# Kernel tuning notes

Measured on AMD Instinct MI355X. Metric: run time of the kernel, lower is better.

The kernel has to match this reference:

```python
import jax, jax.numpy as jnp
import numpy as np

B, N, D, LAT, EC = 1024, 256, 64, 128, 32


def setup_inputs() -> dict:
    key = jax.random.key(0)
    ks = jax.random.split(key, 8)
    s = lambda d: 1.0 / np.sqrt(d)
    return {
        "local_data": jax.random.normal(ks[0], (B, D), jnp.float32),
        "neighbor_data": jax.random.normal(ks[1], (B, N, D), jnp.float32),
        "Wc": jax.random.normal(ks[2], (D, EC), jnp.float32) * s(D),
        "bc": jnp.zeros((EC,), jnp.float32),
        "Wf": jax.random.normal(ks[3], (D, LAT), jnp.float32) * s(D),
        "bf": jnp.zeros((LAT,), jnp.float32),
        "Wa": jax.random.normal(ks[4], (3 * EC, LAT), jnp.float32) * s(3 * EC),
        "ba": jnp.zeros((LAT,), jnp.float32),
        "Wl": jax.random.normal(ks[5], (LAT, LAT), jnp.float32) * s(LAT),
        "bl": jnp.zeros((LAT,), jnp.float32),
    }


def reference(local_data, neighbor_data, Wc, bc, Wf, bf, Wa, ba, Wl, bl):
    # per-neighbor feature encoder: [B,N,LAT]
    enc_feature = jax.nn.relu(jnp.einsum("bnd,dk->bnk", neighbor_data, Wf) + bf)
    # per-neighbor communication encoder: [B,N,EC]
    enc_comm = jax.nn.relu(jnp.einsum("bnd,dk->bnk", neighbor_data, Wc) + bc)
    # self communication embedding: [B,EC]
    enc_comm_self = jax.nn.relu(local_data @ Wc + bc)
    # broadcast self and neighbor-mean to [B,N,EC]
    self_rep = jnp.broadcast_to(enc_comm_self[:, None, :], enc_comm.shape)
    mean_rep = jnp.broadcast_to(enc_comm.mean(axis=1, keepdims=True), enc_comm.shape)
    cat = jnp.concatenate([self_rep, enc_comm, mean_rep], axis=-1)  # [B,N,3*EC]
    # attention: linear then softmax over neighbor axis (dim=-2)
    att = jax.nn.softmax(jnp.einsum("bnc,ck->bnk", cat, Wa) + ba, axis=1)  # [B,N,LAT]
    # attention-weighted sum over neighbors: [B,LAT]
    aggregated = jnp.einsum("bnk,bnk->bk", att, enc_feature)
    # later layer
    return jax.nn.relu(aggregated @ Wl + bl)
```

## Files before the change

kernel.cpp:

```cpp
#include <hip/hip_runtime.h>

#define NB    256
#define DIN   64
#define LATD  128
#define ECD   32

typedef __attribute__((ext_vector_type(8))) __bf16 bf16x8;
typedef __attribute__((ext_vector_type(4))) float f32x4;
typedef __attribute__((ext_vector_type(4))) unsigned short u16x4;

#define XS_STRIDE 72
#define EC_STRIDE 40
#define WA_STRIDE 40

#define WS_WC 0
#define WS_WF (32 * 72)
#define WS_WA (32 * 72 + 128 * 72)

#define MFMA(a, b, c) __builtin_amdgcn_mfma_f32_16x16x32_bf16((a), (b), (c), 0, 0, 0)

__device__ __forceinline__ unsigned short f2bf(float f) {
    unsigned u = __builtin_bit_cast(unsigned, f);
    u += 0x7fffu + ((u >> 16) & 1u);
    return (unsigned short)(u >> 16);
}

__global__ __launch_bounds__(256) void prep_kernel(
    const float* __restrict__ Wc, const float* __restrict__ Wf,
    const float* __restrict__ Wa, unsigned short* __restrict__ ws)
{
    int t = blockIdx.x * blockDim.x + threadIdx.x;
    int stride = gridDim.x * blockDim.x;
    for (int i = t; i < 32 * 64; i += stride) {
        int n = i >> 6, k = i & 63;
        ws[WS_WC + n * XS_STRIDE + k] = f2bf(Wc[k * ECD + n]);
    }
    for (int i = t; i < 128 * 64; i += stride) {
        int n = i >> 6, k = i & 63;
        ws[WS_WF + n * XS_STRIDE + k] = f2bf(Wf[k * LATD + n]);
    }
    for (int i = t; i < 128 * 32; i += stride) {
        int n = i >> 5, k = i & 31;
        ws[WS_WA + n * WA_STRIDE + k] = f2bf(Wa[(ECD + k) * LATD + n]);
    }
}

__global__ __launch_bounds__(256) void arm_main(
    const float* __restrict__ ld,
    const float* __restrict__ xg,
    const float* __restrict__ wc,
    const float* __restrict__ bcv,
    const float* __restrict__ bfv,
    const float* __restrict__ wa,
    const float* __restrict__ bav,
    const float* __restrict__ wl,
    const float* __restrict__ blv,
    const unsigned short* __restrict__ ws,
    float* __restrict__ out)
{
    __shared__ unsigned short Xs[NB * XS_STRIDE];
    __shared__ unsigned short ecs[NB * EC_STRIDE];
    __shared__ float meanpart[4][ECD];
    __shared__ float mean_s[ECD];
    __shared__ float self_s[ECD];
    __shared__ float c0_s[LATD];
    __shared__ float redmax[4][16];
    __shared__ float redsum[4][16];
    __shared__ float aggpart[4][LATD];
    __shared__ float aggfull[LATD];

    const int b    = blockIdx.x;
    const int tid  = threadIdx.x;
    const int lane = tid & 63;
    const int w    = tid >> 6;
    const int l15  = lane & 15;
    const int q    = lane >> 4;

    {
        const float4* xb4 = reinterpret_cast<const float4*>(xg + (size_t)b * NB * DIN);
        #pragma unroll
        for (int i = 0; i < 16; ++i) {
            int i4 = i * 256 + tid;
            float4 v = xb4[i4];
            int n = i4 >> 4;
            int d = (i4 & 15) << 2;
            u16x4 p = { f2bf(v.x), f2bf(v.y), f2bf(v.z), f2bf(v.w) };
            *reinterpret_cast<u16x4*>(&Xs[n * XS_STRIDE + d]) = p;
        }
    }
    __syncthreads();

    {
        bf16x8 wfrag[2][2];
        #pragma unroll
        for (int ks = 0; ks < 2; ++ks)
            #pragma unroll
            for (int nb = 0; nb < 2; ++nb)
                wfrag[ks][nb] = *reinterpret_cast<const bf16x8*>(
                    &ws[WS_WC + (nb * 16 + l15) * XS_STRIDE + ks * 32 + q * 8]);

        float bc0 = bcv[l15], bc1 = bcv[16 + l15];
        float s0 = 0.f, s1 = 0.f;
        #pragma unroll
        for (int t = 0; t < 4; ++t) {
            int rowA = (w * 4 + t) * 16;
            f32x4 a0 = {0.f, 0.f, 0.f, 0.f}, a1 = {0.f, 0.f, 0.f, 0.f};
            #pragma unroll
            for (int ks = 0; ks < 2; ++ks) {
                bf16x8 af = *reinterpret_cast<const bf16x8*>(
                    &Xs[(rowA + l15) * XS_STRIDE + ks * 32 + q * 8]);
                a0 = MFMA(af, wfrag[ks][0], a0);
                a1 = MFMA(af, wfrag[ks][1], a1);
            }
            #pragma unroll
            for (int r = 0; r < 4; ++r) {
                int row = rowA + q * 4 + r;
                float e0 = fmaxf(a0[r] + bc0, 0.f);
                float e1 = fmaxf(a1[r] + bc1, 0.f);
                ecs[row * EC_STRIDE + l15]      = f2bf(e0);
                ecs[row * EC_STRIDE + 16 + l15] = f2bf(e1);
                s0 += e0; s1 += e1;
            }
        }
        s0 += __shfl_xor(s0, 16, 64); s0 += __shfl_xor(s0, 32, 64);
        s1 += __shfl_xor(s1, 16, 64); s1 += __shfl_xor(s1, 32, 64);
        if (lane < 16) { meanpart[w][lane] = s0; meanpart[w][16 + lane] = s1; }
    }
    __syncthreads();

    if (tid < 32) {
        mean_s[tid] = (meanpart[0][tid] + meanpart[1][tid] +
                       meanpart[2][tid] + meanpart[3][tid]) * (1.f / 256.f);
    } else if (tid < 64) {
        int e = tid - 32;
        float acc = 0.f;
        #pragma unroll 8
        for (int d = 0; d < 64; ++d) acc += ld[b * 64 + d] * wc[d * ECD + e];
        self_s[e] = fmaxf(acc + bcv[e], 0.f);
    }
    __syncthreads();

    if (tid < 128) {
        float acc = bav[tid];
        #pragma unroll 4
        for (int e = 0; e < 32; ++e) {
            acc += self_s[e] * wa[e * LATD + tid];
            acc += mean_s[e] * wa[(64 + e) * LATD + tid];
        }
        c0_s[tid] = acc;
    }
    __syncthreads();

    bf16x8 xfrag[4][2];
    bf16x8 ecfrag[4];
    #pragma unroll
    for (int t = 0; t < 4; ++t) {
        int row = (w * 4 + t) * 16 + l15;
        xfrag[t][0] = *reinterpret_cast<const bf16x8*>(&Xs[row * XS_STRIDE + q * 8]);
        xfrag[t][1] = *reinterpret_cast<const bf16x8*>(&Xs[row * XS_STRIDE + 32 + q * 8]);
        ecfrag[t]   = *reinterpret_cast<const bf16x8*>(&ecs[row * EC_STRIDE + q * 8]);
    }

    for (int g = 0; g < 8; ++g) {
        bf16x8 wf0 = *reinterpret_cast<const bf16x8*>(
            &ws[WS_WF + (g * 16 + l15) * XS_STRIDE + q * 8]);
        bf16x8 wf1 = *reinterpret_cast<const bf16x8*>(
            &ws[WS_WF + (g * 16 + l15) * XS_STRIDE + 32 + q * 8]);
        bf16x8 wag = *reinterpret_cast<const bf16x8*>(
            &ws[WS_WA + (g * 16 + l15) * WA_STRIDE + q * 8]);

        f32x4 ef[4], lg[4];
        #pragma unroll
        for (int t = 0; t < 4; ++t) {
            f32x4 z = {0.f, 0.f, 0.f, 0.f};
            z = MFMA(xfrag[t][0], wf0, z);
            ef[t] = MFMA(xfrag[t][1], wf1, z);
            f32x4 z2 = {0.f, 0.f, 0.f, 0.f};
            lg[t] = MFMA(ecfrag[t], wag, z2);
        }
        float bfl = bfv[g * 16 + l15];
        float c0l = c0_s[g * 16 + l15];
        float mx = -1e30f;
        #pragma unroll
        for (int t = 0; t < 4; ++t)
            #pragma unroll
            for (int r = 0; r < 4; ++r) {
                ef[t][r] = fmaxf(ef[t][r] + bfl, 0.f);
                lg[t][r] += c0l;
                mx = fmaxf(mx, lg[t][r]);
            }
        mx = fmaxf(mx, __shfl_xor(mx, 16, 64));
        mx = fmaxf(mx, __shfl_xor(mx, 32, 64));
        if (lane < 16) redmax[w][lane] = mx;
        __syncthreads();
        mx = fmaxf(fmaxf(redmax[0][l15], redmax[1][l15]),
                   fmaxf(redmax[2][l15], redmax[3][l15]));

        float sm = 0.f;
        #pragma unroll
        for (int t = 0; t < 4; ++t)
            #pragma unroll
            for (int r = 0; r < 4; ++r) {
                float e = exp2f((lg[t][r] - mx) * 1.44269504f);
                lg[t][r] = e;
                sm += e;
            }
        sm += __shfl_xor(sm, 16, 64); sm += __shfl_xor(sm, 32, 64);
        if (lane < 16) redsum[w][lane] = sm;
        __syncthreads();
        sm = redsum[0][l15] + redsum[1][l15] + redsum[2][l15] + redsum[3][l15];
        float inv = 1.0f / sm;

        float ag = 0.f;
        #pragma unroll
        for (int t = 0; t < 4; ++t)
            #pragma unroll
            for (int r = 0; r < 4; ++r)
                ag += lg[t][r] * ef[t][r];
        ag *= inv;
        ag += __shfl_xor(ag, 16, 64);
        ag += __shfl_xor(ag, 32, 64);
        if (lane < 16) aggpart[w][g * 16 + lane] = ag;
    }
    __syncthreads();

    if (tid < 128)
        aggfull[tid] = aggpart[0][tid] + aggpart[1][tid] +
                       aggpart[2][tid] + aggpart[3][tid];
    __syncthreads();
    if (tid < 128) {
        float acc = blv[tid];
        #pragma unroll 8
        for (int k = 0; k < 128; ++k) acc += aggfull[k] * wl[k * LATD + tid];
        out[(size_t)b * LATD + tid] = fmaxf(acc, 0.f);
    }
}

extern "C" void kernel_launch(void* const* d_in, const int* in_sizes, int n_in,
                              void* d_out, int out_size, void* d_ws, size_t ws_size,
                              hipStream_t stream)
{
    const float* ld  = (const float*)d_in[0];
    const float* xg  = (const float*)d_in[1];
    const float* wc  = (const float*)d_in[2];
    const float* bc_ = (const float*)d_in[3];
    const float* wf  = (const float*)d_in[4];
    const float* bf_ = (const float*)d_in[5];
    const float* wa  = (const float*)d_in[6];
    const float* ba_ = (const float*)d_in[7];
    const float* wl  = (const float*)d_in[8];
    const float* bl_ = (const float*)d_in[9];
    unsigned short* wsp = (unsigned short*)d_ws;
    float* out = (float*)d_out;

    prep_kernel<<<8, 256, 0, stream>>>(wc, wf, wa, wsp);
    arm_main<<<1024, 256, 0, stream>>>(ld, xg, wc, bc_, bf_, wa, ba_, wl, bl_, wsp, out);
}
```

Before: 149.8 us.

## Drop softmax-invariant attention terms and max pass; load X straight to registers

The self and neighbor-mean logit contributions and the attention bias are constant over the neighbor axis, so they cancel in the softmax and are removed along with their computation. The softmax no longer subtracts a running max. Each wave accumulates numerator and denominator and divides once at the end, which removes two block barriers per output group. Neighbor features are loaded from global memory directly into MFMA register fragments instead of being staged in shared memory, and the final Wl matvec is split across all 256 threads. The missing max subtraction risks exp overflow if logits grow large.

```diff
diff --git a/kernel.cpp b/kernel.cpp
--- a/kernel.cpp
+++ b/kernel.cpp
@@ -7,7 +7,6 @@
 
 typedef __attribute__((ext_vector_type(8))) __bf16 bf16x8;
 typedef __attribute__((ext_vector_type(4))) float f32x4;
-typedef __attribute__((ext_vector_type(4))) unsigned short u16x4;
 
 #define XS_STRIDE 72
 #define EC_STRIDE 40
@@ -23,6 +22,13 @@
     unsigned u = __builtin_bit_cast(unsigned, f);
     u += 0x7fffu + ((u >> 16) & 1u);
     return (unsigned short)(u >> 16);
+}
+
+__device__ __forceinline__ bf16x8 pack8(float4 a, float4 b) {
+    union { unsigned short u[8]; bf16x8 v; } r;
+    r.u[0] = f2bf(a.x); r.u[1] = f2bf(a.y); r.u[2] = f2bf(a.z); r.u[3] = f2bf(a.w);
+    r.u[4] = f2bf(b.x); r.u[5] = f2bf(b.y); r.u[6] = f2bf(b.z); r.u[7] = f2bf(b.w);
+    return r.v;
 }
 
 __global__ __launch_bounds__(256) void prep_kernel(
@@ -45,29 +51,20 @@
     }
 }
 
-__global__ __launch_bounds__(256) void arm_main(
-    const float* __restrict__ ld,
+__global__ __launch_bounds__(256, 4) void arm_main(
     const float* __restrict__ xg,
-    const float* __restrict__ wc,
     const float* __restrict__ bcv,
     const float* __restrict__ bfv,
-    const float* __restrict__ wa,
-    const float* __restrict__ bav,
     const float* __restrict__ wl,
     const float* __restrict__ blv,
     const unsigned short* __restrict__ ws,
     float* __restrict__ out)
 {
-    __shared__ unsigned short Xs[NB * XS_STRIDE];
     __shared__ unsigned short ecs[NB * EC_STRIDE];
-    __shared__ float meanpart[4][ECD];
-    __shared__ float mean_s[ECD];
-    __shared__ float self_s[ECD];
-    __shared__ float c0_s[LATD];
-    __shared__ float redmax[4][16];
-    __shared__ float redsum[4][16];
-    __shared__ float aggpart[4][LATD];
+    __shared__ float aggnum[4][LATD];
+    __shared__ float aggden[4][LATD];
     __shared__ float aggfull[LATD];
+    __shared__ float wlpart[2][LATD];
 
     const int b    = blockIdx.x;
     const int tid  = threadIdx.x;
@@ -76,19 +73,22 @@
     const int l15  = lane & 15;
     const int q    = lane >> 4;
 
-    {
-        const float4* xb4 = reinterpret_cast<const float4*>(xg + (size_t)b * NB * DIN);
-        #pragma unroll
-        for (int i = 0; i < 16; ++i) {
-            int i4 = i * 256 + tid;
-            float4 v = xb4[i4];
-            int n = i4 >> 4;
-            int d = (i4 & 15) << 2;
-            u16x4 p = { f2bf(v.x), f2bf(v.y), f2bf(v.z), f2bf(v.w) };
-            *reinterpret_cast<u16x4*>(&Xs[n * XS_STRIDE + d]) = p;
-        }
-    }
-    __syncthreads();
+    const float* xb = xg + (size_t)b * NB * DIN;
+    float4 st[4][4];
+    #pragma unroll
+    for (int t = 0; t < 4; ++t) {
+        const float* p = xb + (w * 64 + t * 16 + l15) * DIN + q * 8;
+        st[t][0] = *reinterpret_cast<const float4*>(p);
+        st[t][1] = *reinterpret_cast<const float4*>(p + 4);
+        st[t][2] = *reinterpret_cast<const float4*>(p + 32);
+        st[t][3] = *reinterpret_cast<const float4*>(p + 36);
+    }
+    bf16x8 xfrag[4][2];
+    #pragma unroll
+    for (int t = 0; t < 4; ++t) {
+        xfrag[t][0] = pack8(st[t][0], st[t][1]);
+        xfrag[t][1] = pack8(st[t][2], st[t][3]);
+    }
 
     {
         bf16x8 wfrag[2][2];
@@ -100,66 +100,29 @@
                     &ws[WS_WC + (nb * 16 + l15) * XS_STRIDE + ks * 32 + q * 8]);
 
         float bc0 = bcv[l15], bc1 = bcv[16 + l15];
-        float s0 = 0.f, s1 = 0.f;
         #pragma unroll
         for (int t = 0; t < 4; ++t) {
-            int rowA = (w * 4 + t) * 16;
+            int rowA = w * 64 + t * 16;
             f32x4 a0 = {0.f, 0.f, 0.f, 0.f}, a1 = {0.f, 0.f, 0.f, 0.f};
             #pragma unroll
             for (int ks = 0; ks < 2; ++ks) {
-                bf16x8 af = *reinterpret_cast<const bf16x8*>(
-                    &Xs[(rowA + l15) * XS_STRIDE + ks * 32 + q * 8]);
-                a0 = MFMA(af, wfrag[ks][0], a0);
-                a1 = MFMA(af, wfrag[ks][1], a1);
+                a0 = MFMA(xfrag[t][ks], wfrag[ks][0], a0);
+                a1 = MFMA(xfrag[t][ks], wfrag[ks][1], a1);
             }
             #pragma unroll
             for (int r = 0; r < 4; ++r) {
                 int row = rowA + q * 4 + r;
-                float e0 = fmaxf(a0[r] + bc0, 0.f);
-                float e1 = fmaxf(a1[r] + bc1, 0.f);
-                ecs[row * EC_STRIDE + l15]      = f2bf(e0);
-                ecs[row * EC_STRIDE + 16 + l15] = f2bf(e1);
-                s0 += e0; s1 += e1;
+                ecs[row * EC_STRIDE + l15]      = f2bf(fmaxf(a0[r] + bc0, 0.f));
+                ecs[row * EC_STRIDE + 16 + l15] = f2bf(fmaxf(a1[r] + bc1, 0.f));
             }
         }
-        s0 += __shfl_xor(s0, 16, 64); s0 += __shfl_xor(s0, 32, 64);
-        s1 += __shfl_xor(s1, 16, 64); s1 += __shfl_xor(s1, 32, 64);
-        if (lane < 16) { meanpart[w][lane] = s0; meanpart[w][16 + lane] = s1; }
-    }
-    __syncthreads();
-
-    if (tid < 32) {
-        mean_s[tid] = (meanpart[0][tid] + meanpart[1][tid] +
-                       meanpart[2][tid] + meanpart[3][tid]) * (1.f / 256.f);
-    } else if (tid < 64) {
-        int e = tid - 32;
-        float acc = 0.f;
-        #pragma unroll 8
-        for (int d = 0; d < 64; ++d) acc += ld[b * 64 + d] * wc[d * ECD + e];
-        self_s[e] = fmaxf(acc + bcv[e], 0.f);
-    }
-    __syncthreads();
-
-    if (tid < 128) {
-        float acc = bav[tid];
-        #pragma unroll 4
-        for (int e = 0; e < 32; ++e) {
-            acc += self_s[e] * wa[e * LATD + tid];
-            acc += mean_s[e] * wa[(64 + e) * LATD + tid];
-        }
-        c0_s[tid] = acc;
-    }
-    __syncthreads();
-
-    bf16x8 xfrag[4][2];
+    }
+
     bf16x8 ecfrag[4];
     #pragma unroll
-    for (int t = 0; t < 4; ++t) {
-        int row = (w * 4 + t) * 16 + l15;
-        xfrag[t][0] = *reinterpret_cast<const bf16x8*>(&Xs[row * XS_STRIDE + q * 8]);
-        xfrag[t][1] = *reinterpret_cast<const bf16x8*>(&Xs[row * XS_STRIDE + 32 + q * 8]);
-        ecfrag[t]   = *reinterpret_cast<const bf16x8*>(&ecs[row * EC_STRIDE + q * 8]);
-    }
+    for (int t = 0; t < 4; ++t)
+        ecfrag[t] = *reinterpret_cast<const bf16x8*>(
+            &ecs[(w * 64 + t * 16 + l15) * EC_STRIDE + q * 8]);
 
     for (int g = 0; g < 8; ++g) {
         bf16x8 wf0 = *reinterpret_cast<const bf16x8*>(
@@ -179,80 +142,61 @@
             lg[t] = MFMA(ecfrag[t], wag, z2);
         }
         float bfl = bfv[g * 16 + l15];
-        float c0l = c0_s[g * 16 + l15];
-        float mx = -1e30f;
+        float num = 0.f, den = 0.f;
         #pragma unroll
         for (int t = 0; t < 4; ++t)
             #pragma unroll
             for (int r = 0; r < 4; ++r) {
-                ef[t][r] = fmaxf(ef[t][r] + bfl, 0.f);
-                lg[t][r] += c0l;
-                mx = fmaxf(mx, lg[t][r]);
+                float e = fmaxf(ef[t][r] + bfl, 0.f);
+                float p = exp2f(lg[t][r] * 1.44269504f);
+                num += p * e;
+                den += p;
             }
-        mx = fmaxf(mx, __shfl_xor(mx, 16, 64));
-        mx = fmaxf(mx, __shfl_xor(mx, 32, 64));
-        if (lane < 16) redmax[w][lane] = mx;
-        __syncthreads();
-        mx = fmaxf(fmaxf(redmax[0][l15], redmax[1][l15]),
-                   fmaxf(redmax[2][l15], redmax[3][l15]));
-
-        float sm = 0.f;
-        #pragma unroll
-        for (int t = 0; t < 4; ++t)
-            #pragma unroll
-            for (int r = 0; r < 4; ++r) {
-                float e = exp2f((lg[t][r] - mx) * 1.44269504f);
-                lg[t][r] = e;
-                sm += e;
-            }
-        sm += __shfl_xor(sm, 16, 64); sm += __shfl_xor(sm, 32, 64);
-        if (lane < 16) redsum[w][lane] = sm;
-        __syncthreads();
-        sm = redsum[0][l15] + redsum[1][l15] + redsum[2][l15] + redsum[3][l15];
-        float inv = 1.0f / sm;
-
-        float ag = 0.f;
-        #pragma unroll
-        for (int t = 0; t < 4; ++t)
-            #pragma unroll
-            for (int r = 0; r < 4; ++r)
-                ag += lg[t][r] * ef[t][r];
-        ag *= inv;
-        ag += __shfl_xor(ag, 16, 64);
-        ag += __shfl_xor(ag, 32, 64);
-        if (lane < 16) aggpart[w][g * 16 + lane] = ag;
+        num += __shfl_xor(num, 16, 64); num += __shfl_xor(num, 32, 64);
+        den += __shfl_xor(den, 16, 64); den += __shfl_xor(den, 32, 64);
+        if (lane < 16) {
+            aggnum[w][g * 16 + lane] = num;
+            aggden[w][g * 16 + lane] = den;
+        }
     }
     __syncthreads();
 
+    if (tid < 128) {
+        float num = aggnum[0][tid] + aggnum[1][tid] + aggnum[2][tid] + aggnum[3][tid];
+        float den = aggden[0][tid] + aggden[1][tid] + aggden[2][tid] + aggden[3][tid];
+        aggfull[tid] = num / den;
+    }
+    __syncthreads();
+
+    {
+        int c = tid & 127, h = tid >> 7;
+        float acc = 0.f;
+        #pragma unroll 16
+        for (int k = h * 64; k < h * 64 + 64; ++k)
+            acc += aggfull[k] * wl[k * LATD + c];
+        wlpart[h][c] = acc;
+    }
+    __syncthreads();
     if (tid < 128)
-        aggfull[tid] = aggpart[0][tid] + aggpart[1][tid] +
-                       aggpart[2][tid] + aggpart[3][tid];
-    __syncthreads();
-    if (tid < 128) {
-        float acc = blv[tid];
-        #pragma unroll 8
-        for (int k = 0; k < 128; ++k) acc += aggfull[k] * wl[k * LATD + tid];
-        out[(size_t)b * LATD + tid] = fmaxf(acc, 0.f);
-    }
+        out[(size_t)b * LATD + tid] =
+            fmaxf(wlpart[0][tid] + wlpart[1][tid] + blv[tid], 0.f);
 }
 
 extern "C" void kernel_launch(void* const* d_in, const int* in_sizes, int n_in,
                               void* d_out, int out_size, void* d_ws, size_t ws_size,
                               hipStream_t stream)
 {
-    const float* ld  = (const float*)d_in[0];
     const float* xg  = (const float*)d_in[1];
     const float* wc  = (const float*)d_in[2];
     const float* bc_ = (const float*)d_in[3];
     const float* wf  = (const float*)d_in[4];
     const float* bf_ = (const float*)d_in[5];
     const float* wa  = (const float*)d_in[6];
-    const float* ba_ = (const float*)d_in[7];
     const float* wl  = (const float*)d_in[8];
     const float* bl_ = (const float*)d_in[9];
     unsigned short* wsp = (unsigned short*)d_ws;
     float* out = (float*)d_out;
 
     prep_kernel<<<8, 256, 0, stream>>>(wc, wf, wa, wsp);
-    arm_main<<<1024, 256, 0, stream>>>(ld, xg, wc, bc_, bf_, wa, ba_, wl, bl_, wsp, out);
-}
+    arm_main<<<1024, 256, 0, stream>>>(xg, bc_, bf_, wl, bl_, wsp, out);
+}
```

After: 128.6 us. -14.2%, faster.
